# Optimization experiments

Measured on AMD Instinct MI355X. Metric: run time of the kernel, lower is better.

Reference implementation:

```python
import jax, jax.numpy as jnp
import numpy as np

MODEL_DIM = 1024
NUM_HEADS = 16
HEAD_DIM = MODEL_DIM // NUM_HEADS


def _rope(t):
    # t: [B, S, H, hd] -- ESM-style rotary (rotate_half on halves, freqs tiled)
    B, S, H, hd = t.shape
    inv_freq = 1.0 / (10000.0 ** (jnp.arange(0, hd, 2, dtype=jnp.float32) / hd))  # [hd/2]
    freqs = jnp.arange(S, dtype=jnp.float32)[:, None] * inv_freq[None, :]          # [S, hd/2]
    emb = jnp.concatenate([freqs, freqs], axis=-1)                                 # [S, hd]
    cos = jnp.cos(emb)[None, :, None, :].astype(t.dtype)
    sin = jnp.sin(emb)[None, :, None, :].astype(t.dtype)
    t1, t2 = jnp.split(t, 2, axis=-1)
    rot = jnp.concatenate([-t2, t1], axis=-1)
    return t * cos + rot * sin


def setup_inputs() -> dict:
    key = jax.random.key(0)
    ks = jax.random.split(key, 5)
    D = MODEL_DIM
    s = 1.0 / np.sqrt(D)
    return {
        "x": jax.random.normal(ks[0], (2, 2048, D), dtype=jnp.float32),
        "in_proj_w": jax.random.normal(ks[1], (3 * D, D), dtype=jnp.float32) * s,
        "in_proj_b": jax.random.normal(ks[2], (3 * D,), dtype=jnp.float32) * 0.02,
        "out_proj_w": jax.random.normal(ks[3], (D, D), dtype=jnp.float32) * s,
        "out_proj_b": jax.random.normal(ks[4], (D,), dtype=jnp.float32) * 0.02,
    }


def reference(x, in_proj_w, in_proj_b, out_proj_w, out_proj_b):
    B, S, D = x.shape
    H, hd = NUM_HEADS, HEAD_DIM
    # --- manual _in_proj using MHA's packed in_proj params ---
    combined = jnp.einsum('bsd,ed->bse', x, in_proj_w) + in_proj_b  # [B,S,3D]
    q0, k0, v0 = jnp.split(combined, 3, axis=-1)
    # --- rotary on q/k per head ---
    q1 = _rope(q0.reshape(B, S, H, hd)).reshape(B, S, D)
    k1 = _rope(k0.reshape(B, S, H, hd)).reshape(B, S, D)
    # --- nn.MultiheadAttention re-projects q/k/v with the SAME in_proj ---
    Wq, Wk, Wv = in_proj_w[:D], in_proj_w[D:2 * D], in_proj_w[2 * D:]
    bq, bk, bv = in_proj_b[:D], in_proj_b[D:2 * D], in_proj_b[2 * D:]
    q = (jnp.einsum('bsd,ed->bse', q1, Wq) + bq).reshape(B, S, H, hd)
    k = (jnp.einsum('bsd,ed->bse', k1, Wk) + bk).reshape(B, S, H, hd)
    v = (jnp.einsum('bsd,ed->bse', v0, Wv) + bv).reshape(B, S, H, hd)
    # --- scaled dot-product attention ---
    scale = 1.0 / np.sqrt(hd)
    scores = jnp.einsum('bqhd,bkhd->bhqk', q, k) * scale
    attn = jax.nn.softmax(scores, axis=-1)
    ctx = jnp.einsum('bhqk,bkhd->bqhd', attn, v).reshape(B, S, D)
    return jnp.einsum('bsd,ed->bse', ctx, out_proj_w) + out_proj_b
```

## Files before the change

kernel.cpp:

```cpp
#include <hip/hip_runtime.h>
#include <math.h>

#define D_MODEL   1024
#define N_HEADS   16
#define H_DIM     64
#define SEQ       2048
#define BATCH     2
#define ROWS      (BATCH * SEQ)
#define THREE_D   (3 * D_MODEL)

#define QK_SCALE  (0.125f * 1.44269504088896340736f)
#define THR_RAW   (8.0f / QK_SCALE)

typedef __attribute__((ext_vector_type(8))) short short8v;
typedef __attribute__((ext_vector_type(4))) float f32x4;
typedef __attribute__((ext_vector_type(4))) unsigned int uint4v;
typedef __attribute__((ext_vector_type(2))) unsigned int uint2v;

union Frag { uint4v u; short8v s; };

__device__ __forceinline__ void async_copy16(const void* g, void* l)
{
    __builtin_amdgcn_global_load_lds(
        (const __attribute__((address_space(1))) void*)g,
        (__attribute__((address_space(3))) void*)l,
        16, 0, 0);
}

__device__ __forceinline__ int swz8(int row, int oct)
{
    return oct ^ ((row ^ (row >> 2)) & 7);
}

__device__ __forceinline__ uint2v shfl_u2(uint2v v, int src)
{
    uint2v r;
    r.x = (unsigned)__shfl((int)v.x, src);
    r.y = (unsigned)__shfl((int)v.y, src);
    return r;
}

__device__ __forceinline__ void split2x8(const float* v, uint4v& U1, uint4v& U2)
{
    unsigned b1[8], b2[8];
#pragma unroll
    for (int j = 0; j < 8; ++j) {
        const unsigned u = __float_as_uint(v[j]);
        b1[j] = u;
        const float r = v[j] - __uint_as_float(u & 0xFFFF0000u);
        b2[j] = __float_as_uint(r);
    }
    U1 = (uint4v){ (b1[0]>>16)|(b1[1]&0xFFFF0000u), (b1[2]>>16)|(b1[3]&0xFFFF0000u),
                   (b1[4]>>16)|(b1[5]&0xFFFF0000u), (b1[6]>>16)|(b1[7]&0xFFFF0000u) };
    U2 = (uint4v){ (b2[0]>>16)|(b2[1]&0xFFFF0000u), (b2[2]>>16)|(b2[3]&0xFFFF0000u),
                   (b2[4]>>16)|(b2[5]&0xFFFF0000u), (b2[6]>>16)|(b2[7]&0xFFFF0000u) };
}

__device__ __forceinline__ void pack_store(unsigned short* rowp, int col, float val)
{
    unsigned short* d = rowp + ((col >> 5) << 6) + (col & 31);
    const unsigned u = __float_as_uint(val);
    d[0]  = (unsigned short)(u >> 16);
    const float r = val - __uint_as_float(u & 0xFFFF0000u);
    d[32] = (unsigned short)(__float_as_uint(r) >> 16);
}

__global__ __launch_bounds__(256)
void split_pack3(const float* __restrict__ x,    unsigned short* __restrict__ px,
                 const float* __restrict__ w1,   unsigned short* __restrict__ pw1,
                 const float* __restrict__ w2,   unsigned short* __restrict__ pw2)
{
    const int bid = blockIdx.x;
    const float* in;
    unsigned short* out;
    size_t base;
    if (bid < 2048)      { in = x;  out = px;  base = (size_t)bid * 2048; }
    else if (bid < 3584) { in = w1; out = pw1; base = (size_t)(bid - 2048) * 2048; }
    else                 { in = w2; out = pw2; base = (size_t)(bid - 3584) * 2048; }

    const size_t e0 = base + (size_t)threadIdx.x * 8;
    const float4 a0 = *reinterpret_cast<const float4*>(in + e0);
    const float4 a1 = *reinterpret_cast<const float4*>(in + e0 + 4);
    float v[8] = { a0.x, a0.y, a0.z, a0.w, a1.x, a1.y, a1.z, a1.w };
    uint4v U1, U2;
    split2x8(v, U1, U2);
    unsigned short* d = out + ((e0 >> 5) << 6) + (e0 & 31);
    *reinterpret_cast<uint4v*>(d)      = U1;
    *reinterpret_cast<uint4v*>(d + 32) = U2;
}

__global__ void rope_table(float* __restrict__ tab)
{
    const int idx = blockIdx.x * 256 + threadIdx.x;
    const int s = idx >> 5;
    const int i = idx & 31;
    const double inv = pow(10000.0, -(double)(2 * i) / 64.0);
    const double f = (double)s * inv;
    tab[idx * 2 + 0] = (float)cos(f);
    tab[idx * 2 + 1] = (float)sin(f);
}


__global__ __launch_bounds__(256, 2)
void gemm_p(const unsigned short* __restrict__ Ap, int ldA2,
            const unsigned short* __restrict__ Bp, int ldB2,
            const float* __restrict__ bias,
            float* __restrict__ C, int ldc, int K,
            int nbx, size_t segA, size_t segB, int segBias, size_t segC)
{
    __shared__ __align__(16) unsigned short As[2][128 * 64];
    __shared__ __align__(16) unsigned short Bs[2][64 * 64];

    const int fid  = blockIdx.y * gridDim.x + blockIdx.x;
    const int bxpx = gridDim.x >> 3;
    const int xcd  = fid & 7;
    const int idx  = fid >> 3;
    const int bxx  = xcd * bxpx + idx % bxpx;
    const int by   = idx / bxpx;

    const int seg = bxx / nbx;
    const int bxs = bxx - seg * nbx;
    const int bm  = by * 128;
    const int bn  = bxs * 64;
    Ap   += (size_t)seg * segA;
    Bp   += (size_t)seg * segB;
    bias += seg * segBias;
    C    += (size_t)seg * segC;

    const int t    = threadIdx.x;
    const int w    = t >> 6;
    const int lane = t & 63;
    const int cl   = lane & 15;
    const int kq   = lane >> 4;
    const int lrow = lane >> 3;
    const int gs   = lane & 7;

    auto stage = [&](int buf, int k0) {
        const int gl = gs ^ lrow;
#pragma unroll
        for (int q = 0; q < 4; ++q) {
            const int r0  = (w * 4 + q) * 8;
            async_copy16(Ap + (size_t)(bm + r0 + lrow) * ldA2 + (k0 << 1) + (gl << 3),
                         &As[buf][r0 * 64]);
        }
#pragma unroll
        for (int q = 0; q < 2; ++q) {
            const int r0  = (w * 2 + q) * 8;
            async_copy16(Bp + (size_t)(bn + r0 + lrow) * ldB2 + (k0 << 1) + (gl << 3),
                         &Bs[buf][r0 * 64]);
        }
    };

    f32x4 acc[2][4];
#pragma unroll
    for (int m = 0; m < 2; ++m)
#pragma unroll
        for (int n = 0; n < 4; ++n) acc[m][n] = (f32x4)(0.f);

    const int NT = K >> 5;
    stage(0, 0);

    for (int it = 0; it < NT; ++it) {
        __syncthreads();
        if (it + 1 < NT)
            stage((it + 1) & 1, (it + 1) << 5);

        const unsigned short* as = As[it & 1];
        const unsigned short* bs = Bs[it & 1];

        short8v A1[2], A2[2], B1[4], B2[4];
#pragma unroll
        for (int m = 0; m < 2; ++m) {
            const int r = w * 32 + m * 16 + cl;
            const unsigned short* ar = as + r * 64;
            A1[m] = *reinterpret_cast<const short8v*>(ar + (( kq      ^ (r & 7)) << 3));
            A2[m] = *reinterpret_cast<const short8v*>(ar + (((kq + 4) ^ (r & 7)) << 3));
        }
#pragma unroll
        for (int n = 0; n < 4; ++n) {
            const int r = n * 16 + cl;
            const unsigned short* br = bs + r * 64;
            B1[n] = *reinterpret_cast<const short8v*>(br + (( kq      ^ (r & 7)) << 3));
            B2[n] = *reinterpret_cast<const short8v*>(br + (((kq + 4) ^ (r & 7)) << 3));
        }

#pragma unroll
        for (int m = 0; m < 2; ++m)
#pragma unroll
            for (int n = 0; n < 4; ++n) {
                f32x4 c = acc[m][n];
                c = __builtin_amdgcn_mfma_f32_16x16x32_bf16(A1[m], B1[n], c, 0, 0, 0);
                c = __builtin_amdgcn_mfma_f32_16x16x32_bf16(A2[m], B1[n], c, 0, 0, 0);
                c = __builtin_amdgcn_mfma_f32_16x16x32_bf16(A1[m], B2[n], c, 0, 0, 0);
                acc[m][n] = c;
            }
    }

    const int rw = lane >> 4;
#pragma unroll
    for (int n = 0; n < 4; ++n) {
        const int col = bn + n * 16 + cl;
        const float bv = bias[col];
#pragma unroll
        for (int m = 0; m < 2; ++m) {
            const size_t rbase = (size_t)(bm + w * 32 + m * 16 + rw * 4);
#pragma unroll
            for (int i = 0; i < 4; ++i)
                C[(rbase + i) * ldc + col] = acc[m][n][i] + bv;
        }
    }
}

__global__ __launch_bounds__(256, 2)
void gemm_p_pack(const unsigned short* __restrict__ Ap, int ldA2,
                 const unsigned short* __restrict__ Bp, int ldB2,
                 const float* __restrict__ bias,
                 unsigned short* __restrict__ Cp, int ldc2, int K,
                 int nbx, size_t segA, size_t segB, int segBias, size_t segC)
{
    __shared__ __align__(16) unsigned short As[2][128 * 64];
    __shared__ __align__(16) unsigned short Bs[2][64 * 64];

    const int fid  = blockIdx.y * gridDim.x + blockIdx.x;
    const int bxpx = gridDim.x >> 3;
    const int xcd  = fid & 7;
    const int idx  = fid >> 3;
    const int bxx  = xcd * bxpx + idx % bxpx;
    const int by   = idx / bxpx;

    const int seg = bxx / nbx;
    const int bxs = bxx - seg * nbx;
    const int bm  = by * 128;
    const int bn  = bxs * 64;
    Ap   += (size_t)seg * segA;
    Bp   += (size_t)seg * segB;
    bias += seg * segBias;
    Cp   += (size_t)seg * segC;

    const int t    = threadIdx.x;
    const int w    = t >> 6;
    const int lane = t & 63;
    const int cl   = lane & 15;
    const int kq   = lane >> 4;
    const int lrow = lane >> 3;
    const int gs   = lane & 7;

    auto stage = [&](int buf, int k0) {
        const int gl = gs ^ lrow;
#pragma unroll
        for (int q = 0; q < 4; ++q) {
            const int r0  = (w * 4 + q) * 8;
            async_copy16(Ap + (size_t)(bm + r0 + lrow) * ldA2 + (k0 << 1) + (gl << 3),
                         &As[buf][r0 * 64]);
        }
#pragma unroll
        for (int q = 0; q < 2; ++q) {
            const int r0  = (w * 2 + q) * 8;
            async_copy16(Bp + (size_t)(bn + r0 + lrow) * ldB2 + (k0 << 1) + (gl << 3),
                         &Bs[buf][r0 * 64]);
        }
    };

    f32x4 acc[2][4];
#pragma unroll
    for (int m = 0; m < 2; ++m)
#pragma unroll
        for (int n = 0; n < 4; ++n) acc[m][n] = (f32x4)(0.f);

    const int NT = K >> 5;
    stage(0, 0);

    for (int it = 0; it < NT; ++it) {
        __syncthreads();
        if (it + 1 < NT)
            stage((it + 1) & 1, (it + 1) << 5);

        const unsigned short* as = As[it & 1];
        const unsigned short* bs = Bs[it & 1];

        short8v A1[2], A2[2], B1[4], B2[4];
#pragma unroll
        for (int m = 0; m < 2; ++m) {
            const int r = w * 32 + m * 16 + cl;
            const unsigned short* ar = as + r * 64;
            A1[m] = *reinterpret_cast<const short8v*>(ar + (( kq      ^ (r & 7)) << 3));
            A2[m] = *reinterpret_cast<const short8v*>(ar + (((kq + 4) ^ (r & 7)) << 3));
        }
#pragma unroll
        for (int n = 0; n < 4; ++n) {
            const int r = n * 16 + cl;
            const unsigned short* br = bs + r * 64;
            B1[n] = *reinterpret_cast<const short8v*>(br + (( kq      ^ (r & 7)) << 3));
            B2[n] = *reinterpret_cast<const short8v*>(br + (((kq + 4) ^ (r & 7)) << 3));
        }

#pragma unroll
        for (int m = 0; m < 2; ++m)
#pragma unroll
            for (int n = 0; n < 4; ++n) {
                f32x4 c = acc[m][n];
                c = __builtin_amdgcn_mfma_f32_16x16x32_bf16(A1[m], B1[n], c, 0, 0, 0);
                c = __builtin_amdgcn_mfma_f32_16x16x32_bf16(A2[m], B1[n], c, 0, 0, 0);
                c = __builtin_amdgcn_mfma_f32_16x16x32_bf16(A1[m], B2[n], c, 0, 0, 0);
                acc[m][n] = c;
            }
    }

    const int rw = lane >> 4;
#pragma unroll
    for (int n = 0; n < 4; ++n) {
        const int col = bn + n * 16 + cl;
        const float bv = bias[col];
#pragma unroll
        for (int m = 0; m < 2; ++m) {
            const size_t rbase = (size_t)(bm + w * 32 + m * 16 + rw * 4);
#pragma unroll
            for (int i = 0; i < 4; ++i)
                pack_store(Cp + (rbase + i) * (size_t)ldc2, col, acc[m][n][i] + bv);
        }
    }
}

__global__ __launch_bounds__(256, 2)
void gemm_p_rope(const unsigned short* __restrict__ Ap, int ldA2,
                 const unsigned short* __restrict__ Bp, int ldB2,
                 const float* __restrict__ bias,
                 const float* __restrict__ tab,
                 unsigned short* __restrict__ out, int K)
{
    __shared__ __align__(16) unsigned short As[2][128 * 64];
    __shared__ __align__(16) unsigned short Bs[2][64 * 64];

    const int fid  = blockIdx.y * gridDim.x + blockIdx.x;
    const int bxpx = gridDim.x >> 3;
    const int xcd  = fid & 7;
    const int idx  = fid >> 3;
    const int bxx  = xcd * bxpx + idx % bxpx;
    const int by   = idx / bxpx;

    const int bm  = by * 128;
    const int bn  = bxx * 64;

    const int t    = threadIdx.x;
    const int w    = t >> 6;
    const int lane = t & 63;
    const int cl   = lane & 15;
    const int kq   = lane >> 4;
    const int lrow = lane >> 3;
    const int gs   = lane & 7;

    auto stage = [&](int buf, int k0) {
        const int gl = gs ^ lrow;
#pragma unroll
        for (int q = 0; q < 4; ++q) {
            const int r0  = (w * 4 + q) * 8;
            async_copy16(Ap + (size_t)(bm + r0 + lrow) * ldA2 + (k0 << 1) + (gl << 3),
                         &As[buf][r0 * 64]);
        }
#pragma unroll
        for (int q = 0; q < 2; ++q) {
            const int r0  = (w * 2 + q) * 8;
            async_copy16(Bp + (size_t)(bn + r0 + lrow) * ldB2 + (k0 << 1) + (gl << 3),
                         &Bs[buf][r0 * 64]);
        }
    };

    f32x4 acc[2][4];
#pragma unroll
    for (int m = 0; m < 2; ++m)
#pragma unroll
        for (int n = 0; n < 4; ++n) acc[m][n] = (f32x4)(0.f);

    const int NT = K >> 5;
    stage(0, 0);

    for (int it = 0; it < NT; ++it) {
        __syncthreads();
        if (it + 1 < NT)
            stage((it + 1) & 1, (it + 1) << 5);

        const unsigned short* as = As[it & 1];
        const unsigned short* bs = Bs[it & 1];

        short8v A1[2], A2[2], B1[4], B2[4];
#pragma unroll
        for (int m = 0; m < 2; ++m) {
            const int r = w * 32 + m * 16 + cl;
            const unsigned short* ar = as + r * 64;
            A1[m] = *reinterpret_cast<const short8v*>(ar + (( kq      ^ (r & 7)) << 3));
            A2[m] = *reinterpret_cast<const short8v*>(ar + (((kq + 4) ^ (r & 7)) << 3));
        }
#pragma unroll
        for (int n = 0; n < 4; ++n) {
            const int r = n * 16 + cl;
            const unsigned short* br = bs + r * 64;
            B1[n] = *reinterpret_cast<const short8v*>(br + (( kq      ^ (r & 7)) << 3));
            B2[n] = *reinterpret_cast<const short8v*>(br + (((kq + 4) ^ (r & 7)) << 3));
        }

#pragma unroll
        for (int m = 0; m < 2; ++m)
#pragma unroll
            for (int n = 0; n < 4; ++n) {
                f32x4 c = acc[m][n];
                c = __builtin_amdgcn_mfma_f32_16x16x32_bf16(A1[m], B1[n], c, 0, 0, 0);
                c = __builtin_amdgcn_mfma_f32_16x16x32_bf16(A2[m], B1[n], c, 0, 0, 0);
                c = __builtin_amdgcn_mfma_f32_16x16x32_bf16(A1[m], B2[n], c, 0, 0, 0);
                acc[m][n] = c;
            }
    }

    const int rw = lane >> 4;
    const bool doRope = (bn < 2 * D_MODEL);
#pragma unroll
    for (int n = 0; n < 2; ++n) {
        const int colA = bn + n * 16 + cl;
        const int colB = colA + 32;
        const float bvA = bias[colA];
        const float bvB = bias[colB];
        const int d = n * 16 + cl;
#pragma unroll
        for (int m = 0; m < 2; ++m) {
            const size_t rbase = (size_t)(bm + w * 32 + m * 16 + rw * 4);
#pragma unroll
            for (int i = 0; i < 4; ++i) {
                const size_t row = rbase + i;
                const float t1 = acc[m][n][i]     + bvA;
                const float t2 = acc[m][n + 2][i] + bvB;
                float r1 = t1, r2 = t2;
                if (doRope) {
                    const int s = (int)(row & (SEQ - 1));
                    const float c  = tab[(s * 32 + d) * 2 + 0];
                    const float sn = tab[(s * 32 + d) * 2 + 1];
                    r1 = t1 * c - t2 * sn;
                    r2 = t2 * c + t1 * sn;
                }
                unsigned short* op = out + row * (size_t)(THREE_D * 2);
                pack_store(op, colA, r1);
                pack_store(op, colB, r2);
            }
        }
    }
}

__global__ __launch_bounds__(512)
void attn_mfma(const unsigned short* __restrict__ Qp,
               const unsigned short* __restrict__ Kp,
               const unsigned short* __restrict__ Vp,
               unsigned short* __restrict__ pctx)
{
    __shared__ __align__(16) short Ks1[2][64 * 64];
    __shared__ __align__(16) short Vt1[2][64 * 64];
    __shared__ __align__(16) short Vt2[2][64 * 64];

    const int fid = blockIdx.y * gridDim.x + blockIdx.x;
    const int bh  = (fid & 7) * 4 + ((fid >> 3) & 3);
    const int q0  = (fid >> 5) * 128;
    const int b   = bh >> 4;
    const int h   = bh & 15;
    const size_t rowBase = (size_t)b * SEQ;
    const int hs = h * H_DIM * 2;

    const int t    = threadIdx.x;
    const int w    = t >> 6;
    const int lane = t & 63;
    const int cl   = lane & 15;
    const int g    = lane >> 4;
    const int g2   = g >> 1;
    const int srcA = cl + 32 * (g & 1);
    const int srcB = srcA + 16;

    const int krow = t >> 2;
    const int dob  = (t & 3) * 2;
    const int t2   = t - 256;
    const int vkq  = t2 >> 4;
    const int vdq  = t2 & 15;

    const int ksrc = (dob >> 2) * 64 + (dob & 3) * 8;

    Frag qf[2][2];
    {
        const unsigned short* qp =
            Qp + (rowBase + q0 + w * 16 + cl) * (size_t)(D_MODEL * 2) + hs;
#pragma unroll
        for (int c = 0; c < 2; ++c) {
            qf[c][0].u = *reinterpret_cast<const uint4v*>(qp + c * 64 + g * 8);
            qf[c][1].u = *reinterpret_cast<const uint4v*>(qp + c * 64 + 32 + g * 8);
        }
    }

    f32x4 acc[4];
#pragma unroll
    for (int s = 0; s < 4; ++s) acc[s] = (f32x4)(0.f);
    float m = -1e30f;
    float l = 0.f;

    uint4v k1a, k1b;
    uint2v vp1[4], vp2[4];

    auto load_tile = [&](int k0) {
        if (w < 4) {
            const unsigned short* kp =
                Kp + (rowBase + k0 + krow) * (size_t)(D_MODEL * 2) + hs + ksrc;
            k1a = *reinterpret_cast<const uint4v*>(kp);
            k1b = *reinterpret_cast<const uint4v*>(kp + 8);
        } else {
            const unsigned short* vrow =
                Vp + (rowBase + k0 + vkq * 4) * (size_t)(D_MODEL * 2) + hs
                + (((vdq * 4) >> 5) << 6) + ((vdq * 4) & 31);
#pragma unroll
            for (int r = 0; r < 4; ++r) {
                vp1[r] = *reinterpret_cast<const uint2v*>(vrow + r * (D_MODEL * 2));
                vp2[r] = *reinterpret_cast<const uint2v*>(vrow + r * (D_MODEL * 2) + 32);
            }
        }
    };

    auto write_tile = [&](int buf) {
        if (w < 4) {
            short* kb1 = Ks1[buf] + krow * 64;
            *reinterpret_cast<uint4v*>(kb1 + swz8(krow, dob    ) * 8) = k1a;
            *reinterpret_cast<uint4v*>(kb1 + swz8(krow, dob + 1) * 8) = k1b;
        } else {
            const int lo = vkq >> 1;
            const int hf = (vkq & 1) * 4;
#pragma unroll
            for (int rr = 0; rr < 4; ++rr) {
                const int row  = 4 * vdq + rr;
                const int word = rr >> 1;
                const int sh   = (rr & 1) * 16;
                const unsigned e10 = (vp1[0][word] >> sh) & 0xFFFFu;
                const unsigned e11 = (vp1[1][word] >> sh) & 0xFFFFu;
                const unsigned e12 = (vp1[2][word] >> sh) & 0xFFFFu;
                const unsigned e13 = (vp1[3][word] >> sh) & 0xFFFFu;
                const unsigned e20 = (vp2[0][word] >> sh) & 0xFFFFu;
                const unsigned e21 = (vp2[1][word] >> sh) & 0xFFFFu;
                const unsigned e22 = (vp2[2][word] >> sh) & 0xFFFFu;
                const unsigned e23 = (vp2[3][word] >> sh) & 0xFFFFu;
                uint2v w1, w2;
                w1.x = e10 | (e11 << 16);
                w1.y = e12 | (e13 << 16);
                w2.x = e20 | (e21 << 16);
                w2.y = e22 | (e23 << 16);
                const int o = row * 64 + swz8(row, lo) * 8 + hf;
                *reinterpret_cast<uint2v*>(&Vt1[buf][o]) = w1;
                *reinterpret_cast<uint2v*>(&Vt2[buf][o]) = w2;
            }
        }
    };

    const int NT = SEQ / 64;

    load_tile(0);
    write_tile(0);

    for (int it = 0; it < NT; ++it) {
        __syncthreads();
        const int bf = it & 1;
        if (it + 1 < NT)
            load_tile((it + 1) * 64);

        f32x4 sacc[4];
#pragma unroll
        for (int ks = 0; ks < 4; ++ks) sacc[ks] = (f32x4)(0.f);

#pragma unroll
        for (int ks = 0; ks < 4; ++ks)
#pragma unroll
            for (int c = 0; c < 2; ++c) {
                const int row = ks * 16 + cl;
                const int po  = row * 64 + swz8(row, 4 * c + g) * 8;
                Frag ka1;
                ka1.s = *reinterpret_cast<const short8v*>(&Ks1[bf][po]);
                f32x4 s = sacc[ks];
                s = __builtin_amdgcn_mfma_f32_16x16x32_bf16(ka1.s, qf[c][0].s, s, 0, 0, 0);
                s = __builtin_amdgcn_mfma_f32_16x16x32_bf16(ka1.s, qf[c][1].s, s, 0, 0, 0);
                sacc[ks] = s;
            }

        float tm = -1e30f;
#pragma unroll
        for (int ks = 0; ks < 4; ++ks)
#pragma unroll
            for (int i = 0; i < 4; ++i) tm = fmaxf(tm, sacc[ks][i]);
        tm = fmaxf(tm, __shfl_xor(tm, 16));
        tm = fmaxf(tm, __shfl_xor(tm, 32));

        const bool need = !__all(tm <= m + THR_RAW);
        if (need) {
            const float mn = fmaxf(m, tm);
            const float sc = __builtin_amdgcn_exp2f((m - mn) * QK_SCALE);
            m = mn;
            l *= sc;
            float scv[4];
#pragma unroll
            for (int i = 0; i < 4; ++i) scv[i] = __shfl(sc, 4 * g + i);
#pragma unroll
            for (int s = 0; s < 4; ++s)
#pragma unroll
                for (int i = 0; i < 4; ++i) acc[s][i] *= scv[i];
        }
        const float mns = m * QK_SCALE;

        float rs = 0.f;
        uint2v P1[4];
#pragma unroll
        for (int ks = 0; ks < 4; ++ks) {
            float p[4];
            unsigned ub[4];
#pragma unroll
            for (int i = 0; i < 4; ++i) {
                p[i] = __builtin_amdgcn_exp2f(fmaf(sacc[ks][i], QK_SCALE, -mns));
                rs += p[i];
                ub[i] = __float_as_uint(p[i]);
            }
            P1[ks] = (uint2v){ (ub[0] >> 16) | (ub[1] & 0xFFFF0000u),
                               (ub[2] >> 16) | (ub[3] & 0xFFFF0000u) };
        }
        rs += __shfl_xor(rs, 16);
        rs += __shfl_xor(rs, 32);
        l += rs;

#pragma unroll
        for (int c = 0; c < 2; ++c) {
            uint2v a0 = shfl_u2(P1[2 * c],     srcA);
            uint2v a1 = shfl_u2(P1[2 * c + 1], srcA);
            uint2v b0 = shfl_u2(P1[2 * c],     srcB);
            uint2v b1 = shfl_u2(P1[2 * c + 1], srcB);
            uint2v lo = g2 ? a1 : a0;
            uint2v hi = g2 ? b1 : b0;
            Frag pa;
            pa.u = (uint4v){ lo.x, lo.y, hi.x, hi.y };
#pragma unroll
            for (int s = 0; s < 4; ++s) {
                const int row = s * 16 + cl;
                const int vo  = row * 64 + swz8(row, 4 * c + g) * 8;
                Frag vb1, vb2;
                vb1.s = *reinterpret_cast<const short8v*>(&Vt1[bf][vo]);
                vb2.s = *reinterpret_cast<const short8v*>(&Vt2[bf][vo]);
                f32x4 a = acc[s];
                a = __builtin_amdgcn_mfma_f32_16x16x32_bf16(pa.s, vb1.s, a, 0, 0, 0);
                a = __builtin_amdgcn_mfma_f32_16x16x32_bf16(pa.s, vb2.s, a, 0, 0, 0);
                acc[s] = a;
            }
        }

        if (it + 1 < NT)
            write_tile(bf ^ 1);
    }

    const float inv = 1.f / l;
    float iv[4];
#pragma unroll
    for (int i = 0; i < 4; ++i) iv[i] = __shfl(inv, 4 * g + i);
#pragma unroll
    for (int s = 0; s < 4; ++s)
#pragma unroll
        for (int i = 0; i < 4; ++i) {
            const float val = acc[s][i] * iv[i];
            const size_t grow = rowBase + q0 + w * 16 + 4 * g + i;
            const int gc = h * H_DIM + s * 16 + cl;
            pack_store(pctx + grow * (size_t)(D_MODEL * 2), gc, val);
        }
}

extern "C" void kernel_launch(void* const* d_in, const int* in_sizes, int n_in,
                              void* d_out, int out_size, void* d_ws, size_t ws_size,
                              hipStream_t stream)
{
    const float* x    = (const float*)d_in[0];
    const float* Win  = (const float*)d_in[1];
    const float* bin  = (const float*)d_in[2];
    const float* Wout = (const float*)d_in[3];
    const float* bout = (const float*)d_in[4];
    float* out = (float*)d_out;

    float* R1 = (float*)d_ws;
    float* R2 = R1 + (size_t)ROWS * THREE_D;
    unsigned short* pW  = (unsigned short*)(R2 + (size_t)ROWS * THREE_D);
    unsigned short* pWo = pW + (size_t)THREE_D * D_MODEL * 2;
    float* tab = (float*)(pWo + (size_t)D_MODEL * D_MODEL * 2);

    unsigned short* px    = (unsigned short*)R1;
    unsigned short* qkvp  = (unsigned short*)R1;
    unsigned short* pcomb = (unsigned short*)R2;
    unsigned short* pctx  = (unsigned short*)R2;

    unsigned short* Qp = qkvp;
    unsigned short* Kp = qkvp + (size_t)ROWS * D_MODEL * 2;
    unsigned short* Vp = Kp  + (size_t)ROWS * D_MODEL * 2;

    const dim3 blk(256);

    rope_table<<<dim3(SEQ * 32 / 256), blk, 0, stream>>>(tab);

    split_pack3<<<dim3(4096), blk, 0, stream>>>(x, px, Win, pW, Wout, pWo);

    gemm_p_rope<<<dim3(48, 32), blk, 0, stream>>>(
        px, D_MODEL * 2, pW, D_MODEL * 2, bin, tab, pcomb, D_MODEL);

    gemm_p_pack<<<dim3(48, 32), blk, 0, stream>>>(
        pcomb, THREE_D * 2, pW, D_MODEL * 2, bin, qkvp, D_MODEL * 2, D_MODEL,
        16, (size_t)(D_MODEL * 2), (size_t)D_MODEL * D_MODEL * 2, D_MODEL,
        (size_t)ROWS * D_MODEL * 2);

    attn_mfma<<<dim3(SEQ / 128, BATCH * N_HEADS), dim3(512), 0, stream>>>(
        Qp, Kp, Vp, pctx);

    gemm_p<<<dim3(16, 32), blk, 0, stream>>>(
        pctx, D_MODEL * 2, pWo, D_MODEL * 2, bout, out, D_MODEL, D_MODEL,
        16, (size_t)0, (size_t)0, 0, (size_t)0);
}
```

Measured before the change: 300.5 us.

## Split attention KV range across two blocks and merge partials in combine kernel

Splits each attention block's key/value sweep into two halves handled by separate blocks along a new grid z dimension, doubling the number of blocks from 512 to 1024 to improve occupancy across the GPU's compute units. Each half writes unnormalized fp32 accumulators plus running max and sum to workspace. A new combine kernel rescales and merges the two partials, then packs bf16 output. This adds extra global traffic and a kernel launch in exchange for more parallelism.

Result: slower. 354.7 us (+18.0%).

```diff
diff --git a/kernel.cpp b/kernel.cpp
--- a/kernel.cpp
+++ b/kernel.cpp
@@ -447,17 +447,18 @@
 void attn_mfma(const unsigned short* __restrict__ Qp,
                const unsigned short* __restrict__ Kp,
                const unsigned short* __restrict__ Vp,
-               unsigned short* __restrict__ pctx)
+               float* __restrict__ Pacc, float* __restrict__ Pml)
 {
     __shared__ __align__(16) short Ks1[2][64 * 64];
     __shared__ __align__(16) short Vt1[2][64 * 64];
     __shared__ __align__(16) short Vt2[2][64 * 64];
 
-    const int fid = blockIdx.y * gridDim.x + blockIdx.x;
-    const int bh  = (fid & 7) * 4 + ((fid >> 3) & 3);
-    const int q0  = (fid >> 5) * 128;
-    const int b   = bh >> 4;
-    const int h   = bh & 15;
+    const int fid  = blockIdx.y * gridDim.x + blockIdx.x;
+    const int half = blockIdx.z;
+    const int bh   = (fid & 7) * 4 + ((fid >> 3) & 3);
+    const int q0   = (fid >> 5) * 128;
+    const int b    = bh >> 4;
+    const int h    = bh & 15;
     const size_t rowBase = (size_t)b * SEQ;
     const int hs = h * H_DIM * 2;
 
@@ -497,6 +498,8 @@
 
     uint4v k1a, k1b;
     uint2v vp1[4], vp2[4];
+
+    const int kbase = half * (SEQ / 2);
 
     auto load_tile = [&](int k0) {
         if (w < 4) {
@@ -549,16 +552,16 @@
         }
     };
 
-    const int NT = SEQ / 64;
-
-    load_tile(0);
+    const int NT = (SEQ / 2) / 64;
+
+    load_tile(kbase);
     write_tile(0);
 
     for (int it = 0; it < NT; ++it) {
         __syncthreads();
         const int bf = it & 1;
         if (it + 1 < NT)
-            load_tile((it + 1) * 64);
+            load_tile(kbase + (it + 1) * 64);
 
         f32x4 sacc[4];
 #pragma unroll
@@ -649,19 +652,48 @@
             write_tile(bf ^ 1);
     }
 
-    const float inv = 1.f / l;
-    float iv[4];
-#pragma unroll
-    for (int i = 0; i < 4; ++i) iv[i] = __shfl(inv, 4 * g + i);
+    const int pblk = half * 512 + bh * 16 + (q0 >> 7);
+    float* ab = Pacc + (size_t)pblk * (128 * 64);
 #pragma unroll
     for (int s = 0; s < 4; ++s)
 #pragma unroll
-        for (int i = 0; i < 4; ++i) {
-            const float val = acc[s][i] * iv[i];
-            const size_t grow = rowBase + q0 + w * 16 + 4 * g + i;
-            const int gc = h * H_DIM + s * 16 + cl;
-            pack_store(pctx + grow * (size_t)(D_MODEL * 2), gc, val);
-        }
+        for (int i = 0; i < 4; ++i)
+            ab[(w * 16 + 4 * g + i) * 64 + s * 16 + cl] = acc[s][i];
+    if (g == 0) {
+        float2 ml; ml.x = m; ml.y = l;
+        reinterpret_cast<float2*>(Pml)[pblk * 128 + w * 16 + cl] = ml;
+    }
+}
+
+__global__ __launch_bounds__(256)
+void attn_combine(const float* __restrict__ Pacc, const float* __restrict__ Pml,
+                  unsigned short* __restrict__ pctx)
+{
+    const int tid = blockIdx.x * 256 + threadIdx.x;
+    const int col = (tid & 255) * 4;
+    const int row = tid >> 8;
+    const int b = row >> 11, s = row & 2047;
+    const int h = col >> 6,  d = col & 63;
+    const int p0 = (b * 16 + h) * 16 + (s >> 7);
+    const int q  = s & 127;
+
+    const float2 mlA = reinterpret_cast<const float2*>(Pml)[p0 * 128 + q];
+    const float2 mlB = reinterpret_cast<const float2*>(Pml)[(p0 + 512) * 128 + q];
+    const float4 a = *reinterpret_cast<const float4*>(
+        Pacc + ((size_t)p0 * 128 + q) * 64 + d);
+    const float4 c = *reinterpret_cast<const float4*>(
+        Pacc + ((size_t)(p0 + 512) * 128 + q) * 64 + d);
+
+    const float mf = fmaxf(mlA.x, mlB.x);
+    const float wa = __builtin_amdgcn_exp2f((mlA.x - mf) * QK_SCALE);
+    const float wb = __builtin_amdgcn_exp2f((mlB.x - mf) * QK_SCALE);
+    const float inv = 1.f / (wa * mlA.y + wb * mlB.y);
+
+    unsigned short* op = pctx + (size_t)row * (D_MODEL * 2);
+    pack_store(op, col + 0, (wa * a.x + wb * c.x) * inv);
+    pack_store(op, col + 1, (wa * a.y + wb * c.y) * inv);
+    pack_store(op, col + 2, (wa * a.z + wb * c.z) * inv);
+    pack_store(op, col + 3, (wa * a.w + wb * c.w) * inv);
 }
 
 extern "C" void kernel_launch(void* const* d_in, const int* in_sizes, int n_in,
@@ -680,11 +712,13 @@
     unsigned short* pW  = (unsigned short*)(R2 + (size_t)ROWS * THREE_D);
     unsigned short* pWo = pW + (size_t)THREE_D * D_MODEL * 2;
     float* tab = (float*)(pWo + (size_t)D_MODEL * D_MODEL * 2);
+    float* Pml = tab + (size_t)SEQ * 64;
 
     unsigned short* px    = (unsigned short*)R1;
     unsigned short* qkvp  = (unsigned short*)R1;
     unsigned short* pcomb = (unsigned short*)R2;
     unsigned short* pctx  = (unsigned short*)R2;
+    float* Pacc = R2 + (size_t)ROWS * D_MODEL;
 
     unsigned short* Qp = qkvp;
     unsigned short* Kp = qkvp + (size_t)ROWS * D_MODEL * 2;
@@ -704,8 +738,9 @@
         16, (size_t)(D_MODEL * 2), (size_t)D_MODEL * D_MODEL * 2, D_MODEL,
         (size_t)ROWS * D_MODEL * 2);
 
-    attn_mfma<<<dim3(SEQ / 128, BATCH * N_HEADS), dim3(512), 0, stream>>>(
-        Qp, Kp, Vp, pctx);
+    attn_mfma<<<dim3(16, 32, 2), dim3(512), 0, stream>>>(
+        Qp, Kp, Vp, Pacc, Pml);
+    attn_combine<<<dim3(ROWS), blk, 0, stream>>>(Pacc, Pml, pctx);
 
     gemm_p<<<dim3(16, 32), blk, 0, stream>>>(
         pctx, D_MODEL * 2, pWo, D_MODEL * 2, bout, out, D_MODEL, D_MODEL,
```
